# Optimization experiments

Measured on AMD Instinct MI355X. Metric: run time of the kernel, lower is better.

Reference implementation:

```python
import jax, jax.numpy as jnp
from jax import lax
import numpy as np

B, H, W, C = 8, 64, 64, 128   # NHWC input
F = 256                        # output filters
KH = KW = 3
K = KH * KW
DG = 1                         # deformable groups
CG = C // DG                   # channels per deformable group
PAD_Y, PAD_X = (KH - 1) // 2, (KW - 1) // 2  # SAME padding, stride 1, dilation 1


def setup_inputs() -> dict:
    k1, k2, k3 = jax.random.split(jax.random.key(0), 3)
    return {
        "inputs": jax.random.normal(k1, (B, H, W, C), jnp.float32),
        # conv_offset: Conv2D(dg*3*kh*kw, kernel_size, padding='same', use_bias=True)
        "offset_kernel": jax.random.normal(k2, (KH, KW, C, DG * 3 * K), jnp.float32) * 0.01,
        "offset_bias": jnp.zeros((DG * 3 * K,), jnp.float32),
        # main filter, HWIO as built for channels_last
        "filt": jax.random.normal(k3, (KH, KW, C, F), jnp.float32) * 0.05,
    }


def _deform_conv2d(inputs, offset_kernel, offset_bias, filt):
    # 1) predict offsets + modulation mask with a plain conv (stride 1, SAME)
    wi = lax.conv_general_dilated(
        inputs, offset_kernel, (1, 1), "SAME",
        dimension_numbers=("NHWC", "HWIO", "NHWC")) + offset_bias
    o1, o2, m = jnp.split(wi, 3, axis=-1)           # each [B,H,W,DG*K]
    mask = jax.nn.sigmoid(m).reshape(B, H, W, DG, K)

    # 2) sampling coordinates: base conv grid + learned offsets (o1 = y, o2 = x)
    ky, kx = jnp.meshgrid(jnp.arange(KH), jnp.arange(KW), indexing="ij")
    base_y = (jnp.arange(H)[:, None] - PAD_Y + ky.reshape(-1)[None, :]).astype(jnp.float32)  # [H,K]
    base_x = (jnp.arange(W)[:, None] - PAD_X + kx.reshape(-1)[None, :]).astype(jnp.float32)  # [W,K]
    py = base_y[None, :, None, None, :] + o1.reshape(B, H, W, DG, K)  # [B,H,W,DG,K]
    px = base_x[None, None, :, None, :] + o2.reshape(B, H, W, DG, K)

    # 3) modulated bilinear sampling with zero padding outside the image
    img = inputs.reshape(B, H, W, DG, CG)
    y0f = jnp.floor(py)
    x0f = jnp.floor(px)
    wy1 = py - y0f
    wy0 = 1.0 - wy1
    wx1 = px - x0f
    wx0 = 1.0 - wx1
    bidx = jnp.arange(B)[:, None, None, None, None]
    gidx = jnp.arange(DG)[None, None, None, :, None]

    def corner(yf, xf, wgt):
        valid = (yf >= 0) & (yf <= H - 1) & (xf >= 0) & (xf <= W - 1)
        yi = jnp.clip(yf, 0, H - 1).astype(jnp.int32)
        xi = jnp.clip(xf, 0, W - 1).astype(jnp.int32)
        v = img[bidx, yi, xi, gidx]                  # [B,H,W,DG,K,CG]
        return v * (wgt * valid.astype(jnp.float32))[..., None]

    sampled = (corner(y0f, x0f, wy0 * wx0)
               + corner(y0f, x0f + 1.0, wy0 * wx1)
               + corner(y0f + 1.0, x0f, wy1 * wx0)
               + corner(y0f + 1.0, x0f + 1.0, wy1 * wx1))
    sampled = sampled * mask[..., None]              # DCNv2 modulation

    # 4) im2col columns -> GEMM with the main filter (num_groups = 1)
    cols = jnp.moveaxis(sampled, 3, 4).reshape(B, H, W, K, C)  # channels dg-major
    return jnp.einsum("bhwkc,kcf->bhwf", cols, filt.reshape(K, C, F))


def reference(inputs, offset_kernel, offset_bias, filt):
    return _deform_conv2d(inputs, offset_kernel, offset_bias, filt)
```

## Files before the change

kernel.cpp:

```cpp
#include <hip/hip_runtime.h>
#include <hip/hip_fp16.h>
#include <math.h>

#define B_  8
#define H_  64
#define W_  64
#define C_  128
#define F_  256
#define NOC 27

typedef float    f32x4 __attribute__((ext_vector_type(4)));
typedef _Float16 f16x8 __attribute__((ext_vector_type(8)));

#define FILTT_OFF_F 32768
#define INH_OFF_F   1228800
#define AIM_OFF_F   3325952

static __device__ __forceinline__ unsigned pkh2(float a, float b) {
    __half2 h = __floats2half2_rn(a, b);
    union { __half2 h2; unsigned u; } cv; cv.h2 = h;
    return cv.u;
}

static __device__ __forceinline__ void async16(void* lds, const void* g) {
    __builtin_amdgcn_global_load_lds(
        (const __attribute__((address_space(1))) unsigned int*)g,
        (__attribute__((address_space(3))) unsigned int*)lds, 16, 0, 0);
}

__global__ __launch_bounds__(256) void prep(const float* __restrict__ kofs,
                                            const float* __restrict__ filt,
                                            const float* __restrict__ in,
                                            unsigned short* __restrict__ woffT,
                                            unsigned short* __restrict__ filtT2,
                                            unsigned short* __restrict__ inh) {
    int bidx = blockIdx.x;
    if (bidx >= 1296) {
        int gid = (bidx - 1296) * 256 + threadIdx.x;
        const float4* ip = reinterpret_cast<const float4*>(in) + (size_t)gid * 4;
        float4 a = ip[0], b = ip[1], c = ip[2], d = ip[3];
        uint4 r0 = make_uint4(pkh2(a.x, a.y), pkh2(a.z, a.w), pkh2(b.x, b.y), pkh2(b.z, b.w));
        uint4 r1 = make_uint4(pkh2(c.x, c.y), pkh2(c.z, c.w), pkh2(d.x, d.y), pkh2(d.z, d.w));
        uint4* op = reinterpret_cast<uint4*>(inh) + (size_t)gid * 2;
        op[0] = r0; op[1] = r1;
        return;
    }
    int idx = bidx * 256 + threadIdx.x;
    if (idx < 9 * 32 * 128) {
        int tap = idx >> 12;
        int r   = idx & 4095;
        int oc  = r >> 7;
        int c   = r & 127;
        float v = (oc < NOC) ? kofs[(tap * C_ + c) * NOC + oc] : 0.f;
        union { __half h; unsigned short u; } cv; cv.h = __float2half(v);
        woffT[idx] = cv.u;
        return;
    }
    int idx2 = idx - 9 * 32 * 128;
    if (idx2 < 9 * 256 * 128) {
        int tap = idx2 / 32768;
        int r   = idx2 & 32767;
        int f   = r >> 7;
        int c   = r & 127;
        float v = filt[(tap * C_ + c) * F_ + f];
        union { __half h; unsigned short u; } cv; cv.h = __float2half(v);
        filtT2[(size_t)f * 1152 + tap * 128 + c] = cv.u;
    }
}

__global__ __launch_bounds__(256) void sample_row(const unsigned short* __restrict__ inh,
                                                  const unsigned short* __restrict__ woffT,
                                                  const float* __restrict__ bias,
                                                  unsigned short* __restrict__ Aim) {
    __shared__ float wi[64][33];
    __shared__ __align__(16) uint4 prmo[64][9];
    __shared__ __align__(16) uint2 prmw[64][9];

    int t    = threadIdx.x;
    int bid  = blockIdx.x;
    int lg   = ((bid & 7) << 6) | (bid >> 3);
    int bb   = lg >> 6;
    int hh   = lg & 63;
    int pix0 = lg << 6;

    const char* ih = (const char*)inh;

    {
        int lane = t & 63, wv = t >> 6;
        int row  = lane & 15, kg = lane >> 4;
        int px0  = wv << 4;

        f32x4 z = {0.f, 0.f, 0.f, 0.f};
        f32x4 acc[2] = {z, z};

        #pragma unroll 1
        for (int tap = 0; tap < 9; ++tap) {
            int ky = tap / 3, kx = tap - ky * 3;
            int y  = hh + ky - 1;
            int xg = px0 + row + kx - 1;
            bool ok = ((unsigned)y < 64u) && ((unsigned)xg < 64u);
            int pix = (bb << 12) + (y << 6) + xg;
            const char* ap = ih + ((long long)pix << 8) + (kg << 4);
            const unsigned short* bp = woffT + (size_t)tap * 4096 + (size_t)row * 128 + kg * 8;
            union { uint4 u; f16x8 v; } a[4];
            #pragma unroll
            for (int ks = 0; ks < 4; ++ks) {
                uint4 av = *(const uint4*)(ap + (ks << 6));
                a[ks].u = ok ? av : make_uint4(0u, 0u, 0u, 0u);
            }
            #pragma unroll
            for (int ks = 0; ks < 4; ++ks) {
                f16x8 b0 = *(const f16x8*)(bp + ks * 32);
                f16x8 b1 = *(const f16x8*)(bp + 2048 + ks * 32);
                acc[0] = __builtin_amdgcn_mfma_f32_16x16x32_f16(a[ks].v, b0, acc[0], 0, 0, 0);
                acc[1] = __builtin_amdgcn_mfma_f32_16x16x32_f16(a[ks].v, b1, acc[1], 0, 0, 0);
            }
        }
        #pragma unroll
        for (int n = 0; n < 2; ++n) {
            int oc = n * 16 + row;
            float bv = (oc < NOC) ? bias[oc] : 0.f;
            #pragma unroll
            for (int r = 0; r < 4; ++r)
                wi[px0 + kg * 4 + r][oc] = acc[n][r] + bv;
        }
    }
    __syncthreads();

    for (int it = t; it < 576; it += 256) {
        int px  = it & 63;
        int tap = it >> 6;
        float o1 = wi[px][tap], o2 = wi[px][9 + tap], mm = wi[px][18 + tap];
        float mask = 1.f / (1.f + __expf(-mm));
        int ky = tap / 3, kx = tap - ky * 3;
        float py  = (float)(hh - 1 + ky) + o1;
        float pxx = (float)(px - 1 + kx) + o2;
        float y0f = floorf(py), x0f = floorf(pxx);
        float wy1 = py - y0f,  wy0 = 1.f - wy1;
        float wx1 = pxx - x0f, wx0 = 1.f - wx1;
        float vy0 = (y0f >=  0.f && y0f <= 63.f) ? 1.f : 0.f;
        float vy1 = (y0f >= -1.f && y0f <= 62.f) ? 1.f : 0.f;
        float vx0 = (x0f >=  0.f && x0f <= 63.f) ? 1.f : 0.f;
        float vx1 = (x0f >= -1.f && x0f <= 62.f) ? 1.f : 0.f;
        int y0 = (int)fminf(fmaxf(y0f,       0.f), 63.f);
        int y1 = (int)fminf(fmaxf(y0f + 1.f, 0.f), 63.f);
        int x0 = (int)fminf(fmaxf(x0f,       0.f), 63.f);
        int x1 = (int)fminf(fmaxf(x0f + 1.f, 0.f), 63.f);
        int base = bb << 12;
        prmo[px][tap] = make_uint4((unsigned)((base + (y0 << 6) + x0) << 8),
                                   (unsigned)((base + (y0 << 6) + x1) << 8),
                                   (unsigned)((base + (y1 << 6) + x0) << 8),
                                   (unsigned)((base + (y1 << 6) + x1) << 8));
        prmw[px][tap] = make_uint2(pkh2(wy0 * wx0 * mask * vy0 * vx0,
                                        wy0 * wx1 * mask * vy0 * vx1),
                                   pkh2(wy1 * wx0 * mask * vy1 * vx0,
                                        wy1 * wx1 * mask * vy1 * vx1));
    }
    __syncthreads();

    int c8  = t & 15;
    int pxg = (t >> 4) & 7;
    int th  = t >> 7;
    int cb  = c8 << 4;

    int tbeg = th ? 5 : 0, tend = th ? 9 : 5;
    union AU { uint4 u; __half2 h[4]; };

    #pragma unroll 2
    for (int pp = 0; pp < 8; ++pp) {
        int px = pxg + (pp << 3);
        char* Ao = (char*)Aim + (size_t)(pix0 + px) * 2304;
        #pragma unroll 5
        for (int tap = tbeg; tap < tend; ++tap) {
            uint4 O  = prmo[px][tap];
            uint2 Wp = prmw[px][tap];
            union { unsigned u; __half2 h; } w00, w01, w10, w11;
            w00.u = (Wp.x & 0xFFFFu) * 0x10001u;
            w01.u = (Wp.x >> 16)     * 0x10001u;
            w10.u = (Wp.y & 0xFFFFu) * 0x10001u;
            w11.u = (Wp.y >> 16)     * 0x10001u;
            AU c00, c01, c10, c11, s;
            c00.u = *(const uint4*)(ih + O.x + cb);
            c01.u = *(const uint4*)(ih + O.y + cb);
            c10.u = *(const uint4*)(ih + O.z + cb);
            c11.u = *(const uint4*)(ih + O.w + cb);
            #pragma unroll
            for (int j = 0; j < 4; ++j) {
                __half2 sj = __hmul2(c00.h[j], w00.h);
                sj = __hfma2(c01.h[j], w01.h, sj);
                sj = __hfma2(c10.h[j], w10.h, sj);
                s.h[j] = __hfma2(c11.h[j], w11.h, sj);
            }
            *(uint4*)(Ao + tap * 256 + cb) = s.u;
        }
    }
}

__global__ __launch_bounds__(256) void gemm_im2col(const unsigned short* __restrict__ Aim,
                                                   const unsigned short* __restrict__ filtT2,
                                                   float* __restrict__ out) {
    __shared__ __align__(16) unsigned char As[2][16384];
    __shared__ __align__(16) unsigned char Bs[2][16384];

    int t   = threadIdx.x;
    int bid = blockIdx.x;
    int lg  = ((bid & 7) << 6) | (bid >> 3);
    int mt  = lg >> 1, nt = lg & 1;
    int apix = mt << 7;
    int f0   = nt << 7;

    int lane = t & 63, wv = t >> 6;
    int wm = wv & 1, wn = wv >> 1;
    int row16 = lane & 15, kg = lane >> 4;

    const char* Ab = (const char*)Aim;
    const char* Bb = (const char*)filtT2;

    f32x4 z = {0.f, 0.f, 0.f, 0.f};
    f32x4 acc[4][4];
    #pragma unroll
    for (int m = 0; m < 4; ++m)
        #pragma unroll
        for (int n = 0; n < 4; ++n) acc[m][n] = z;

    int lin0 = wv * 1024 + lane * 16;

    auto stageTo = [&](unsigned char* A, unsigned char* B, int s) {
        int k2 = s << 7;
        #pragma unroll
        for (int it = 0; it < 4; ++it) {
            int lin = lin0 + it * 4096;
            int r_  = lin >> 7;
            int c_  = (lin & 127) ^ ((r_ & 7) << 4);
            async16(A + wv * 1024 + it * 4096,
                    Ab + (size_t)(apix + r_) * 2304 + k2 + c_);
            async16(B + wv * 1024 + it * 4096,
                    Bb + (size_t)(f0 + r_) * 2304 + k2 + c_);
        }
    };

    auto mfmaOn = [&](const unsigned char* A, const unsigned char* B) {
        int sw = (row16 & 7) << 4;
        #pragma unroll
        for (int ks = 0; ks < 2; ++ks) {
            int kcol = ((ks << 6) + (kg << 4)) ^ sw;
            f16x8 a[4], b[4];
            #pragma unroll
            for (int m = 0; m < 4; ++m)
                a[m] = *(const f16x8*)(A + ((wm << 6) + (m << 4) + row16) * 128 + kcol);
            #pragma unroll
            for (int n = 0; n < 4; ++n)
                b[n] = *(const f16x8*)(B + ((wn << 6) + (n << 4) + row16) * 128 + kcol);
            #pragma unroll
            for (int m = 0; m < 4; ++m)
                #pragma unroll
                for (int n = 0; n < 4; ++n)
                    acc[m][n] = __builtin_amdgcn_mfma_f32_16x16x32_f16(a[m], b[n], acc[m][n], 0, 0, 0);
        }
    };

    stageTo(As[0], Bs[0], 0);
    __syncthreads();

    #pragma unroll 1
    for (int kb = 0; kb < 18; kb += 2) {
        stageTo(As[1], Bs[1], kb + 1);
        mfmaOn(As[0], Bs[0]);
        __syncthreads();
        if (kb < 16) stageTo(As[0], Bs[0], kb + 2);
        mfmaOn(As[1], Bs[1]);
        __syncthreads();
    }

    int pxb = apix + (wm << 6);
    int fcb = f0 + (wn << 6) + row16;
    #pragma unroll
    for (int m = 0; m < 4; ++m)
        #pragma unroll
        for (int r = 0; r < 4; ++r) {
            int px = pxb + (m << 4) + (kg << 2) + r;
            float* op = out + (size_t)px * 256 + fcb;
            op[0]  = acc[m][0][r];
            op[16] = acc[m][1][r];
            op[32] = acc[m][2][r];
            op[48] = acc[m][3][r];
        }
}

extern "C" void kernel_launch(void* const* d_in, const int* in_sizes, int n_in,
                              void* d_out, int out_size, void* d_ws, size_t ws_size,
                              hipStream_t stream) {
    const float* in   = (const float*)d_in[0];
    const float* kofs = (const float*)d_in[1];
    const float* bias = (const float*)d_in[2];
    const float* filt = (const float*)d_in[3];
    float* out = (float*)d_out;
    float* ws  = (float*)d_ws;

    unsigned short* woffT  = (unsigned short*)ws;
    unsigned short* filtT2 = (unsigned short*)(ws + FILTT_OFF_F);
    unsigned short* inh    = (unsigned short*)(ws + INH_OFF_F);
    unsigned short* Aim    = (unsigned short*)(ws + AIM_OFF_F);

    hipLaunchKernelGGL(prep, dim3(2320), dim3(256), 0, stream, kofs, filt, in, woffT, filtT2, inh);
    hipLaunchKernelGGL(sample_row, dim3(512), dim3(256), 0, stream, inh, woffT, bias, Aim);
    hipLaunchKernelGGL(gemm_im2col, dim3(512), dim3(256), 0, stream, Aim, filtT2, out);
}
```

Before: 77.44 us.

## Split sampling kernel into 16-pixel blocks for more parallelism

Replaces the per-row sampling kernel (512 blocks of 64 pixels) with one that handles 16 pixels per block across 2048 blocks. Only one wave computes the offset-conv MFMA and 144 threads compute the sampling parameters, while all 256 threads do the bilinear gather with one pixel and 16 channels per thread over 9 taps. The aim is more blocks in flight to hide gather latency and a shorter serial offset-conv phase per block. In exchange, three of four waves sit idle during the MFMA phase, and each block has more sync and setup overhead relative to its work.

```diff
diff --git a/kernel.cpp b/kernel.cpp
--- a/kernel.cpp
+++ b/kernel.cpp
@@ -68,28 +68,26 @@
     }
 }
 
-__global__ __launch_bounds__(256) void sample_row(const unsigned short* __restrict__ inh,
-                                                  const unsigned short* __restrict__ woffT,
-                                                  const float* __restrict__ bias,
-                                                  unsigned short* __restrict__ Aim) {
-    __shared__ float wi[64][33];
-    __shared__ __align__(16) uint4 prmo[64][9];
-    __shared__ __align__(16) uint2 prmw[64][9];
+__global__ __launch_bounds__(256) void sample16(const unsigned short* __restrict__ inh,
+                                                const unsigned short* __restrict__ woffT,
+                                                const float* __restrict__ bias,
+                                                unsigned short* __restrict__ Aim) {
+    __shared__ float wi[16][33];
+    __shared__ __align__(16) uint4 prmo[16][9];
+    __shared__ __align__(16) uint2 prmw[16][9];
 
     int t    = threadIdx.x;
     int bid  = blockIdx.x;
-    int lg   = ((bid & 7) << 6) | (bid >> 3);
-    int bb   = lg >> 6;
-    int hh   = lg & 63;
-    int pix0 = lg << 6;
+    int lg   = ((bid & 7) << 8) | (bid >> 3);
+    int pix0 = lg << 4;
+    int bb   = pix0 >> 12;
+    int hh   = (pix0 >> 6) & 63;
+    int col0 = pix0 & 63;
 
     const char* ih = (const char*)inh;
 
-    {
-        int lane = t & 63, wv = t >> 6;
-        int row  = lane & 15, kg = lane >> 4;
-        int px0  = wv << 4;
-
+    if (t < 64) {
+        int row = t & 15, kg = t >> 4;
         f32x4 z = {0.f, 0.f, 0.f, 0.f};
         f32x4 acc[2] = {z, z};
 
@@ -97,7 +95,7 @@
         for (int tap = 0; tap < 9; ++tap) {
             int ky = tap / 3, kx = tap - ky * 3;
             int y  = hh + ky - 1;
-            int xg = px0 + row + kx - 1;
+            int xg = col0 + row + kx - 1;
             bool ok = ((unsigned)y < 64u) && ((unsigned)xg < 64u);
             int pix = (bb << 12) + (y << 6) + xg;
             const char* ap = ih + ((long long)pix << 8) + (kg << 4);
@@ -122,19 +120,19 @@
             float bv = (oc < NOC) ? bias[oc] : 0.f;
             #pragma unroll
             for (int r = 0; r < 4; ++r)
-                wi[px0 + kg * 4 + r][oc] = acc[n][r] + bv;
+                wi[kg * 4 + r][oc] = acc[n][r] + bv;
         }
     }
     __syncthreads();
 
-    for (int it = t; it < 576; it += 256) {
-        int px  = it & 63;
-        int tap = it >> 6;
+    if (t < 144) {
+        int px  = t & 15;
+        int tap = t >> 4;
         float o1 = wi[px][tap], o2 = wi[px][9 + tap], mm = wi[px][18 + tap];
         float mask = 1.f / (1.f + __expf(-mm));
         int ky = tap / 3, kx = tap - ky * 3;
         float py  = (float)(hh - 1 + ky) + o1;
-        float pxx = (float)(px - 1 + kx) + o2;
+        float pxx = (float)(col0 + px - 1 + kx) + o2;
         float y0f = floorf(py), x0f = floorf(pxx);
         float wy1 = py - y0f,  wy0 = 1.f - wy1;
         float wx1 = pxx - x0f, wx0 = 1.f - wx1;
@@ -158,41 +156,35 @@
     }
     __syncthreads();
 
-    int c8  = t & 15;
-    int pxg = (t >> 4) & 7;
-    int th  = t >> 7;
-    int cb  = c8 << 4;
-
-    int tbeg = th ? 5 : 0, tend = th ? 9 : 5;
+    int c8 = t & 15;
+    int px = t >> 4;
+    int cb = c8 << 4;
+
+    char* Ao = (char*)Aim + (size_t)(pix0 + px) * 2304 + cb;
     union AU { uint4 u; __half2 h[4]; };
 
-    #pragma unroll 2
-    for (int pp = 0; pp < 8; ++pp) {
-        int px = pxg + (pp << 3);
-        char* Ao = (char*)Aim + (size_t)(pix0 + px) * 2304;
-        #pragma unroll 5
-        for (int tap = tbeg; tap < tend; ++tap) {
-            uint4 O  = prmo[px][tap];
-            uint2 Wp = prmw[px][tap];
-            union { unsigned u; __half2 h; } w00, w01, w10, w11;
-            w00.u = (Wp.x & 0xFFFFu) * 0x10001u;
-            w01.u = (Wp.x >> 16)     * 0x10001u;
-            w10.u = (Wp.y & 0xFFFFu) * 0x10001u;
-            w11.u = (Wp.y >> 16)     * 0x10001u;
-            AU c00, c01, c10, c11, s;
-            c00.u = *(const uint4*)(ih + O.x + cb);
-            c01.u = *(const uint4*)(ih + O.y + cb);
-            c10.u = *(const uint4*)(ih + O.z + cb);
-            c11.u = *(const uint4*)(ih + O.w + cb);
-            #pragma unroll
-            for (int j = 0; j < 4; ++j) {
-                __half2 sj = __hmul2(c00.h[j], w00.h);
-                sj = __hfma2(c01.h[j], w01.h, sj);
-                sj = __hfma2(c10.h[j], w10.h, sj);
-                s.h[j] = __hfma2(c11.h[j], w11.h, sj);
-            }
-            *(uint4*)(Ao + tap * 256 + cb) = s.u;
-        }
+    #pragma unroll 3
+    for (int tap = 0; tap < 9; ++tap) {
+        uint4 O  = prmo[px][tap];
+        uint2 Wp = prmw[px][tap];
+        union { unsigned u; __half2 h; } w00, w01, w10, w11;
+        w00.u = (Wp.x & 0xFFFFu) * 0x10001u;
+        w01.u = (Wp.x >> 16)     * 0x10001u;
+        w10.u = (Wp.y & 0xFFFFu) * 0x10001u;
+        w11.u = (Wp.y >> 16)     * 0x10001u;
+        AU c00, c01, c10, c11, s;
+        c00.u = *(const uint4*)(ih + O.x + cb);
+        c01.u = *(const uint4*)(ih + O.y + cb);
+        c10.u = *(const uint4*)(ih + O.z + cb);
+        c11.u = *(const uint4*)(ih + O.w + cb);
+        #pragma unroll
+        for (int j = 0; j < 4; ++j) {
+            __half2 sj = __hmul2(c00.h[j], w00.h);
+            sj = __hfma2(c01.h[j], w01.h, sj);
+            sj = __hfma2(c10.h[j], w10.h, sj);
+            s.h[j] = __hfma2(c11.h[j], w11.h, sj);
+        }
+        *(uint4*)(Ao + tap * 256) = s.u;
     }
 }
 
@@ -303,6 +295,6 @@
     unsigned short* Aim    = (unsigned short*)(ws + AIM_OFF_F);
 
     hipLaunchKernelGGL(prep, dim3(2320), dim3(256), 0, stream, kofs, filt, in, woffT, filtT2, inh);
-    hipLaunchKernelGGL(sample_row, dim3(512), dim3(256), 0, stream, inh, woffT, bias, Aim);
+    hipLaunchKernelGGL(sample16, dim3(2048), dim3(256), 0, stream, inh, woffT, bias, Aim);
     hipLaunchKernelGGL(gemm_im2col, dim3(512), dim3(256), 0, stream, Aim, filtT2, out);
 }
```

Result: no change. 76.69 us (-1.0%).
